# Kernel tuning notes

Measured on AMD Instinct MI355X. Metric: run time of the kernel, lower is better.

## Reference

```python
import jax, jax.numpy as jnp
import numpy as np

LN_EPS = 1e-5


def layer_norm(x, w, b):
    mu = jnp.mean(x, axis=-1, keepdims=True)
    var = jnp.mean(jnp.square(x - mu), axis=-1, keepdims=True)
    return (x - mu) * jax.lax.rsqrt(var + LN_EPS) * w + b


def setup_inputs() -> dict:
    key = jax.random.key(0)
    ks = jax.random.split(key, 10)
    B, S, D, H, DH, F = 2, 2048, 1024, 16, 64, 4096

    def xavier(k, shape):
        fan_in, fan_out = shape[-1], int(np.prod(shape[:-1]))
        lim = float(np.sqrt(6.0 / (fan_in + fan_out)))
        return jax.random.uniform(k, shape, jnp.float32, -lim, lim)

    x = jax.random.normal(ks[0], (B, S, D), jnp.float32)
    W_Q = xavier(ks[1], (H, DH, D))
    W_K = xavier(ks[2], (H, DH, D))
    W_V = xavier(ks[3], (H, DH, D))
    W_O = xavier(ks[4], (D, DH, H))
    mlp_w1 = jax.random.normal(ks[5], (F, D), jnp.float32) * (1.0 / np.sqrt(D))
    mlp_b1 = jnp.zeros((F,), jnp.float32)
    mlp_w2 = jax.random.normal(ks[6], (D, F), jnp.float32) * (1.0 / np.sqrt(F))
    mlp_b2 = jnp.zeros((D,), jnp.float32)
    ln_att_w = jnp.ones((D,), jnp.float32)
    ln_att_b = jnp.zeros((D,), jnp.float32)
    ln_mlp_w = jnp.ones((D,), jnp.float32)
    ln_mlp_b = jnp.zeros((D,), jnp.float32)
    return dict(x=x, W_Q=W_Q, W_K=W_K, W_V=W_V, W_O=W_O,
                ln_att_w=ln_att_w, ln_att_b=ln_att_b,
                ln_mlp_w=ln_mlp_w, ln_mlp_b=ln_mlp_b,
                mlp_w1=mlp_w1, mlp_b1=mlp_b1, mlp_w2=mlp_w2, mlp_b2=mlp_b2)


def reference(x, W_Q, W_K, W_V, W_O, ln_att_w, ln_att_b, ln_mlp_w, ln_mlp_b,
              mlp_w1, mlp_b1, mlp_w2, mlp_b2):
    B, S, D = x.shape
    d_head = W_Q.shape[1]
    y = layer_norm(x, ln_att_w, ln_att_b)
    Q = jnp.einsum('ihd,bpd->biph', W_Q, y)  # [B,H,S,dh]
    K = jnp.einsum('ihd,bpd->biph', W_K, y)
    V = jnp.einsum('ihd,bpd->biph', W_V, y)
    scores = jnp.einsum('biph,biqh->biqp', K, Q)  # [B,H,q,p]
    causal = jnp.tril(jnp.ones((S, S), jnp.bool_))  # True where attended
    masked = scores - 1e10 * (~causal).astype(scores.dtype)
    att = jax.nn.softmax(masked / np.sqrt(d_head), axis=-1)
    z = jnp.einsum('biph,biqp->biqh', V, att)
    x_att = jnp.einsum('dhi,biqh->bqd', W_O, z)
    x = x + x_att
    y2 = layer_norm(x, ln_mlp_w, ln_mlp_b)
    h = jax.nn.relu(y2 @ mlp_w1.T + mlp_b1)
    x = x + (h @ mlp_w2.T + mlp_b2)
    return x, att
```

## Files before the change

### kernel.cpp

```cpp
#include <hip/hip_runtime.h>
#include <hip/hip_bf16.h>
#include <stdint.h>

typedef __attribute__((ext_vector_type(8))) short bf16x8;
typedef __attribute__((ext_vector_type(4))) short short4v;
typedef __attribute__((ext_vector_type(4))) float f32x4;

#define GLOAD16(g, s) __builtin_amdgcn_global_load_lds( \
    (const __attribute__((address_space(1))) void*)(g),  \
    (__attribute__((address_space(3))) void*)(s), 16, 0, 0)

static __device__ __forceinline__ short f2bf(float f) {
  unsigned u = __builtin_bit_cast(unsigned, f);
  u += 0x7fffu + ((u >> 16) & 1u);
  return (short)(u >> 16);
}

static __device__ __forceinline__ f32x4 mfma16(bf16x8 a, bf16x8 b, f32x4 c) {
  return __builtin_amdgcn_mfma_f32_16x16x32_bf16(a, b, c, 0, 0, 0);
}

__global__ __launch_bounds__(256) void cvt_all(
    const float* __restrict__ WQ, const float* __restrict__ WK,
    const float* __restrict__ WV, const float* __restrict__ WO,
    const float* __restrict__ w1, const float* __restrict__ w2,
    short* __restrict__ Wqkv, short* __restrict__ Wob,
    short* __restrict__ w1b, short* __restrict__ w2b) {
  const int bi = blockIdx.x, tid = threadIdx.x;
  if (bi < 3072) {
    const float* src = bi < 1024 ? WQ : (bi < 2048 ? WK : WV);
    const float4 v = ((const float4*)(src + (size_t)(bi & 1023) * 1024))[tid];
    short4v o;
    o[0] = f2bf(v.x); o[1] = f2bf(v.y); o[2] = f2bf(v.z); o[3] = f2bf(v.w);
    ((short4v*)(Wqkv + (size_t)bi * 1024))[tid] = o;
  } else if (bi < 7168) {
    const int i = (bi - 3072) * 256 + tid;
    const float4 v = ((const float4*)w1)[i];
    short4v o;
    o[0] = f2bf(v.x); o[1] = f2bf(v.y); o[2] = f2bf(v.z); o[3] = f2bf(v.w);
    ((short4v*)w1b)[i] = o;
  } else if (bi < 11264) {
    const int i = (bi - 7168) * 256 + tid;
    const float4 v = ((const float4*)w2)[i];
    short4v o;
    o[0] = f2bf(v.x); o[1] = f2bf(v.y); o[2] = f2bf(v.z); o[3] = f2bf(v.w);
    ((short4v*)w2b)[i] = o;
  } else {
    const int idx = (bi - 11264) * 256 + tid;
    const int d = idx >> 10, cc = idx & 1023;
    const int i = cc >> 6, h = cc & 63;
    Wob[idx] = f2bf(WO[((size_t)d * 64 + h) * 16 + i]);
  }
}

__global__ __launch_bounds__(256) void ln_kernel(const float* __restrict__ x,
                                                 const float* __restrict__ w,
                                                 const float* __restrict__ b,
                                                 short* __restrict__ y) {
  const int row = blockIdx.x, tid = threadIdx.x;
  const int lane = tid & 63, wave = tid >> 6;
  const float4 xv = *(const float4*)&x[(size_t)row * 1024 + tid * 4];
  float s1 = xv.x + xv.y + xv.z + xv.w;
  float s2 = xv.x * xv.x + xv.y * xv.y + xv.z * xv.z + xv.w * xv.w;
#pragma unroll
  for (int off = 1; off < 64; off <<= 1) {
    s1 += __shfl_xor(s1, off);
    s2 += __shfl_xor(s2, off);
  }
  __shared__ float red[8];
  if (lane == 0) { red[wave] = s1; red[4 + wave] = s2; }
  __syncthreads();
  s1 = red[0] + red[1] + red[2] + red[3];
  s2 = red[4] + red[5] + red[6] + red[7];
  const float mu = s1 * (1.0f / 1024.0f);
  const float var = s2 * (1.0f / 1024.0f) - mu * mu;
  const float rs = rsqrtf(var + 1e-5f);
  const float4 wv = *(const float4*)&w[tid * 4];
  const float4 bv = *(const float4*)&b[tid * 4];
  short4v o;
  o[0] = f2bf((xv.x - mu) * rs * wv.x + bv.x);
  o[1] = f2bf((xv.y - mu) * rs * wv.y + bv.y);
  o[2] = f2bf((xv.z - mu) * rs * wv.z + bv.z);
  o[3] = f2bf((xv.w - mu) * rs * wv.w + bv.w);
  *(short4v*)&y[(size_t)row * 1024 + tid * 4] = o;
}

template <int MODE, int BM, int BN>
__global__ __launch_bounds__(256) void gemm_bf16k(
    const short* __restrict__ A, const short* __restrict__ Bw,
    float* __restrict__ outF, short* __restrict__ outB,
    const float* __restrict__ resid, const float* __restrict__ bias,
    int M, int N, int K) {
  constexpr int RBM = BM / 2, RBN = BN / 2;
  constexpr int FM = RBM / 16, FN = RBN / 16;
  constexpr int TCA = BM / 8, TCB = BN / 8, TC = TCA + TCB;
  __shared__ short As[BM * 64];
  __shared__ short Bs[BN * 64];
  const int tid = threadIdx.x, lane = tid & 63, wave = tid >> 6;
  const int nbx = gridDim.x, nwg = nbx * gridDim.y;
  int lid = (int)blockIdx.y * nbx + (int)blockIdx.x;
  lid = (lid & 7) * (nwg >> 3) + (lid >> 3);
  const int m0 = (lid / nbx) * BM, n0 = (lid % nbx) * BN;
  const int wm = (wave & 1) * RBM, wn = (wave >> 1) * RBN;
  const int lr = lane >> 3;
  const int lc = (lane & 7) * 8;
  f32x4 acc[FM][FN] = {};

  for (int kt = 0; kt < K; kt += 64) {
#pragma unroll
    for (int i = 0; i < TC / 4; ++i) {
      const int ch = i * 4 + wave;
      if (ch < TCA) {
        const short* ga = A + (size_t)(m0 + ch * 8 + lr) * K + kt + lc;
        GLOAD16(ga, &As[ch * 512]);
      } else {
        const int cb = ch - TCA;
        const short* gb = Bw + (size_t)(n0 + cb * 8 + lr) * K + kt + lc;
        GLOAD16(gb, &Bs[cb * 512]);
      }
    }
    __syncthreads();
#pragma unroll
    for (int kk = 0; kk < 64; kk += 32) {
      bf16x8 af[FM], bfr[FN];
#pragma unroll
      for (int i2 = 0; i2 < FM; ++i2)
        af[i2] = *(const bf16x8*)&As[(wm + i2 * 16 + (lane & 15)) * 64 + kk + (lane >> 4) * 8];
#pragma unroll
      for (int j2 = 0; j2 < FN; ++j2)
        bfr[j2] = *(const bf16x8*)&Bs[(wn + j2 * 16 + (lane & 15)) * 64 + kk + (lane >> 4) * 8];
#pragma unroll
      for (int i2 = 0; i2 < FM; ++i2)
#pragma unroll
        for (int j2 = 0; j2 < FN; ++j2)
          acc[i2][j2] = mfma16(af[i2], bfr[j2], acc[i2][j2]);
    }
    __syncthreads();
  }

#pragma unroll
  for (int i2 = 0; i2 < FM; ++i2)
#pragma unroll
    for (int j2 = 0; j2 < FN; ++j2)
#pragma unroll
      for (int r = 0; r < 4; ++r) {
        const int m = m0 + wm + i2 * 16 + (lane >> 4) * 4 + r;
        const int n = n0 + wn + j2 * 16 + (lane & 15);
        const float v = acc[i2][j2][r];
        if (MODE == 0) {
          const size_t oi = (size_t)(n >> 10) * 4194304 +
              ((size_t)((m >> 11) * 16 + ((n & 1023) >> 6)) * 2048 + (m & 2047)) * 64 +
              (n & 63);
          outB[oi] = f2bf(v);
        } else if (MODE == 1) {
          outF[(size_t)m * N + n] = resid[(size_t)m * N + n] + v;
        } else if (MODE == 2) {
          const float t2 = v + bias[n];
          outB[(size_t)m * N + n] = f2bf(t2 > 0.0f ? t2 : 0.0f);
        } else {
          outF[(size_t)m * N + n] = resid[(size_t)m * N + n] + v + bias[n];
        }
      }
}

__global__ __launch_bounds__(256) void transpose_v(const short* __restrict__ V,
                                                   short* __restrict__ Vt) {
  __shared__ short t[64][72];
  const int bi = blockIdx.y;
  const int p0 = blockIdx.x * 64;
  const short* Vh = V + (size_t)bi * 2048 * 64;
  short* Vth = Vt + (size_t)bi * 64 * 2048;
  const int tid = threadIdx.x;
  {
    const int pr = tid >> 2, h0 = (tid & 3) * 16;
    const bf16x8* src = (const bf16x8*)&Vh[(size_t)(p0 + pr) * 64 + h0];
    bf16x8 v0 = src[0], v1 = src[1];
#pragma unroll
    for (int j = 0; j < 8; ++j) { t[pr][h0 + j] = v0[j]; t[pr][h0 + 8 + j] = v1[j]; }
  }
  __syncthreads();
  {
    const int hr = tid >> 2, pq = (tid & 3) * 16;
    bf16x8 o0, o1;
#pragma unroll
    for (int j = 0; j < 8; ++j) { o0[j] = t[pq + j][hr]; o1[j] = t[pq + 8 + j][hr]; }
    *(bf16x8*)&Vth[(size_t)hr * 2048 + p0 + pq] = o0;
    *(bf16x8*)&Vth[(size_t)hr * 2048 + p0 + pq + 8] = o1;
  }
}

__global__ __launch_bounds__(256, 2) void attn_flash(
    const short* __restrict__ Q, const short* __restrict__ K,
    const short* __restrict__ Vt, float* __restrict__ ml,
    short* __restrict__ zb) {
  __shared__ __align__(16) char smem[34816];
  const int tid = threadIdx.x, lane = tid & 63, pc = tid >> 6;
  const int g = lane >> 4, c = lane & 15;
  const int qt = 63 - (int)blockIdx.x;
  const int bi = blockIdx.y;
  const int b = bi >> 4, hd = bi & 15;
  const size_t hoff = (size_t)bi * 2048 * 64;
  const short* Qh = Q + hoff;
  const short* Kh = K + hoff;
  const short* Vth = Vt + hoff;
  short* zbh = zb + (size_t)b * 2048 * 1024 + hd * 64;

  const int qw = qt * 32;
  const int P = qw + 32;
  const int csz = ((P + 511) >> 9) << 7;
  const int p_lo = pc * csz;
  const int p_hi = min(p_lo + csz, P);

  short* pbuf = (short*)smem + pc * 4224;
  float* mlb  = (float*)(smem + 33792);
  float* zm   = (float*)smem;

  const bf16x8* qp0 = (const bf16x8*)&Qh[(size_t)(qw + c) * 64];
  const bf16x8* qp1 = (const bf16x8*)&Qh[(size_t)(qw + 16 + c) * 64];
  bf16x8 aq[2][2];
  aq[0][0] = qp0[g]; aq[0][1] = qp0[4 + g];
  aq[1][0] = qp1[g]; aq[1][1] = qp1[4 + g];

  float m4[2][4], l4[2][4];
  f32x4 zacc[2][4] = {};
#pragma unroll
  for (int rb = 0; rb < 2; ++rb)
#pragma unroll
    for (int r = 0; r < 4; ++r) { m4[rb][r] = -1e30f; l4[rb][r] = 0.0f; }

  for (int p0 = p_lo; p0 < p_hi; p0 += 128) {
    bf16x8 k0[8], k1[8];
#pragma unroll
    for (int kb = 0; kb < 8; ++kb) {
      int row = p0 + kb * 16 + c;
      row = row < 2047 ? row : 2047;
      const bf16x8* kp = (const bf16x8*)&Kh[(size_t)row * 64];
      k0[kb] = kp[g]; k1[kb] = kp[4 + g];
    }
    const bool needmask = (p0 + 128 > qw);
#pragma unroll
    for (int rb = 0; rb < 2; ++rb) {
      f32x4 s[8];
#pragma unroll
      for (int kb = 0; kb < 8; ++kb) {
        f32x4 z4 = {0.0f, 0.0f, 0.0f, 0.0f};
        z4 = mfma16(aq[rb][0], k0[kb], z4);
        s[kb] = mfma16(aq[rb][1], k1[kb], z4);
      }
#pragma unroll
      for (int r = 0; r < 4; ++r) {
        const int q = qw + rb * 16 + g * 4 + r;
        float v[8];
        if (needmask) {
#pragma unroll
          for (int kb = 0; kb < 8; ++kb)
            v[kb] = (p0 + kb * 16 + c <= q) ? s[kb][r] * 0.125f : -1e30f;
        } else {
#pragma unroll
          for (int kb = 0; kb < 8; ++kb) v[kb] = s[kb][r] * 0.125f;
        }
        float mx = fmaxf(fmaxf(fmaxf(v[0], v[1]), fmaxf(v[2], v[3])),
                         fmaxf(fmaxf(v[4], v[5]), fmaxf(v[6], v[7])));
#pragma unroll
        for (int off = 1; off < 16; off <<= 1)
          mx = fmaxf(mx, __shfl_xor(mx, off));
        const float mn = fmaxf(m4[rb][r], mx);
        const float fac = __expf(m4[rb][r] - mn);
        m4[rb][r] = mn;
        float lsum = 0.0f;
        if (needmask) {
#pragma unroll
          for (int kb = 0; kb < 8; ++kb) {
            const int p = p0 + kb * 16 + c;
            const float e = (p <= q) ? __expf(v[kb] - mn) : 0.0f;
            lsum += e;
            pbuf[(rb * 16 + g * 4 + r) * 132 + kb * 16 + c] = f2bf(e);
          }
        } else {
#pragma unroll
          for (int kb = 0; kb < 8; ++kb) {
            const float e = __expf(v[kb] - mn);
            lsum += e;
            pbuf[(rb * 16 + g * 4 + r) * 132 + kb * 16 + c] = f2bf(e);
          }
        }
        l4[rb][r] = l4[rb][r] * fac + lsum;
#pragma unroll
        for (int hb = 0; hb < 4; ++hb) zacc[rb][hb][r] *= fac;
      }
    }
#pragma unroll
    for (int j = 0; j < 4; ++j) {
      const short4v p0lo = *(const short4v*)&pbuf[c * 132 + j * 32 + g * 8];
      const short4v p0hi = *(const short4v*)&pbuf[c * 132 + j * 32 + g * 8 + 4];
      const short4v p1lo = *(const short4v*)&pbuf[(16 + c) * 132 + j * 32 + g * 8];
      const short4v p1hi = *(const short4v*)&pbuf[(16 + c) * 132 + j * 32 + g * 8 + 4];
      const bf16x8 pa0 = __builtin_shufflevector(p0lo, p0hi, 0, 1, 2, 3, 4, 5, 6, 7);
      const bf16x8 pa1 = __builtin_shufflevector(p1lo, p1hi, 0, 1, 2, 3, 4, 5, 6, 7);
#pragma unroll
      for (int hb = 0; hb < 4; ++hb) {
        const bf16x8 bv =
            *(const bf16x8*)&Vth[(size_t)(hb * 16 + c) * 2048 + p0 + j * 32 + g * 8];
        zacc[0][hb] = mfma16(pa0, bv, zacc[0][hb]);
        zacc[1][hb] = mfma16(pa1, bv, zacc[1][hb]);
      }
    }
  }

#pragma unroll
  for (int rb = 0; rb < 2; ++rb)
#pragma unroll
    for (int r = 0; r < 4; ++r)
#pragma unroll
      for (int off = 1; off < 16; off <<= 1)
        l4[rb][r] += __shfl_xor(l4[rb][r], off);

  if (c == 0) {
#pragma unroll
    for (int rb = 0; rb < 2; ++rb)
#pragma unroll
      for (int r = 0; r < 4; ++r) {
        mlb[(pc * 32 + rb * 16 + g * 4 + r) * 2 + 0] = m4[rb][r];
        mlb[(pc * 32 + rb * 16 + g * 4 + r) * 2 + 1] = l4[rb][r];
      }
  }
  __syncthreads();

  if (pc != 0) {
#pragma unroll
    for (int rb = 0; rb < 2; ++rb)
#pragma unroll
      for (int hb = 0; hb < 4; ++hb)
#pragma unroll
        for (int r = 0; r < 4; ++r)
          zm[((pc - 1) * 32 + rb * 16 + g * 4 + r) * 68 + hb * 16 + c] = zacc[rb][hb][r];
  }
  __syncthreads();
  if (pc == 0) {
#pragma unroll
    for (int rb = 0; rb < 2; ++rb)
#pragma unroll
      for (int r = 0; r < 4; ++r) {
        const int row = rb * 16 + g * 4 + r;
        float M = -1e30f;
#pragma unroll
        for (int j = 0; j < 4; ++j) M = fmaxf(M, mlb[(j * 32 + row) * 2 + 0]);
        float w[4], L = 0.0f;
#pragma unroll
        for (int j = 0; j < 4; ++j) {
          w[j] = __expf(mlb[(j * 32 + row) * 2 + 0] - M);
          L += mlb[(j * 32 + row) * 2 + 1] * w[j];
        }
        const float iL = 1.0f / L;
#pragma unroll
        for (int hb = 0; hb < 4; ++hb) {
          float z = zacc[rb][hb][r] * w[0];
#pragma unroll
          for (int j = 1; j < 4; ++j)
            z += zm[((j - 1) * 32 + row) * 68 + hb * 16 + c] * w[j];
          zbh[(size_t)(qw + row) * 1024 + hb * 16 + c] = f2bf(z * iL);
        }
        if (c == 0)
          ((float2*)ml)[(size_t)bi * 2048 + qw + row] = make_float2(M, iL);
      }
  }
}

__global__ __launch_bounds__(256) void att_write(
    const short* __restrict__ Q, const short* __restrict__ K,
    const float* __restrict__ ml, float* __restrict__ att) {
  __shared__ float fbuf_s[4][16 * 36];
  const int tid = threadIdx.x, lane = tid & 63, wave = tid >> 6;
  const int g = lane >> 4, c = lane & 15;
  const int qt = blockIdx.x, pt = blockIdx.y, bi = blockIdx.z;
  const int qs = wave >> 1, ph = wave & 1;
  const int qw = qt * 32 + qs * 16;
  const int pb = pt * 256 + ph * 128;
  float* atth = att + (size_t)bi * 2048 * 2048;
  const int r0 = lane >> 3, c4 = (lane & 7) * 4;

  if (pb > qw + 15) {
    const f32x4 zf = {0.0f, 0.0f, 0.0f, 0.0f};
#pragma unroll
    for (int j = 0; j < 4; ++j) {
      __builtin_nontemporal_store(zf, (f32x4*)&atth[(size_t)(qw + r0) * 2048 + pb + j * 32 + c4]);
      __builtin_nontemporal_store(zf, (f32x4*)&atth[(size_t)(qw + 8 + r0) * 2048 + pb + j * 32 + c4]);
    }
    return;
  }

  const size_t hoff = (size_t)bi * 2048 * 64;
  const short* Qh = Q + hoff;
  const short* Kh = K + hoff;
  const bf16x8* qp = (const bf16x8*)&Qh[(size_t)(qw + c) * 64];
  const bf16x8 aq0 = qp[g], aq1 = qp[4 + g];
  float m4[4], il[4];
#pragma unroll
  for (int r = 0; r < 4; ++r) {
    const float2 t = ((const float2*)ml)[(size_t)bi * 2048 + qw + g * 4 + r];
    m4[r] = t.x; il[r] = t.y;
  }
  float* fbuf = fbuf_s[wave];
  for (int p0 = pb; p0 < pb + 128; p0 += 32) {
    const bf16x8* kp0 = (const bf16x8*)&Kh[(size_t)(p0 + c) * 64];
    const bf16x8* kp1 = (const bf16x8*)&Kh[(size_t)(p0 + 16 + c) * 64];
    f32x4 s0 = {0.0f, 0.0f, 0.0f, 0.0f}, s1 = {0.0f, 0.0f, 0.0f, 0.0f};
    s0 = mfma16(aq0, kp0[g], s0);
    s0 = mfma16(aq1, kp0[4 + g], s0);
    s1 = mfma16(aq0, kp1[g], s1);
    s1 = mfma16(aq1, kp1[4 + g], s1);
#pragma unroll
    for (int f = 0; f < 2; ++f) {
      const f32x4& ss = f ? s1 : s0;
#pragma unroll
      for (int r = 0; r < 4; ++r) {
        const int q = qw + g * 4 + r, p = p0 + f * 16 + c;
        const float e = (p <= q) ? __expf(ss[r] * 0.125f - m4[r]) * il[r] : 0.0f;
        fbuf[(g * 4 + r) * 36 + f * 16 + c] = e;
      }
    }
    const f32x4 v0 = *(const f32x4*)&fbuf[r0 * 36 + c4];
    const f32x4 v1 = *(const f32x4*)&fbuf[(8 + r0) * 36 + c4];
    __builtin_nontemporal_store(v0, (f32x4*)&atth[(size_t)(qw + r0) * 2048 + p0 + c4]);
    __builtin_nontemporal_store(v1, (f32x4*)&atth[(size_t)(qw + 8 + r0) * 2048 + p0 + c4]);
  }
}

extern "C" void kernel_launch(void* const* d_in, const int* in_sizes, int n_in,
                              void* d_out, int out_size, void* d_ws, size_t ws_size,
                              hipStream_t stream) {
  (void)in_sizes; (void)n_in; (void)out_size; (void)ws_size;
  const float* x    = (const float*)d_in[0];
  const float* WQ   = (const float*)d_in[1];
  const float* WK   = (const float*)d_in[2];
  const float* WV   = (const float*)d_in[3];
  const float* WO   = (const float*)d_in[4];
  const float* lnaw = (const float*)d_in[5];
  const float* lnab = (const float*)d_in[6];
  const float* lnmw = (const float*)d_in[7];
  const float* lnmb = (const float*)d_in[8];
  const float* w1   = (const float*)d_in[9];
  const float* b1   = (const float*)d_in[10];
  const float* w2   = (const float*)d_in[11];
  const float* b2   = (const float*)d_in[12];

  char* ws = (char*)d_ws;
  const size_t MB = 1024 * 1024;
  short* Wqkv = (short*)(ws + 0 * MB);
  short* Wob  = (short*)(ws + 6 * MB);
  short* w1b  = (short*)(ws + 8 * MB);
  short* w2b  = (short*)(ws + 16 * MB);
  short* yb   = (short*)(ws + 24 * MB);
  short* Qb   = (short*)(ws + 32 * MB);
  short* Kb   = (short*)(ws + 40 * MB);
  short* Vb   = (short*)(ws + 48 * MB);
  short* Vtb  = (short*)(ws + 56 * MB);
  short* zbuf = (short*)(ws + 64 * MB);
  float* x1   = (float*)(ws + 72 * MB);
  float* mlw  = (float*)(ws + 72 * MB);
  short* hb   = (short*)(ws + 32 * MB);

  float* outx = (float*)d_out;
  float* att  = outx + (size_t)2 * 2048 * 1024;

  cvt_all<<<dim3(15360), dim3(256), 0, stream>>>(WQ, WK, WV, WO, w1, w2,
                                                 Wqkv, Wob, w1b, w2b);

  ln_kernel<<<dim3(4096), dim3(256), 0, stream>>>(x, lnaw, lnab, yb);

  gemm_bf16k<0, 128, 128><<<dim3(24, 32), dim3(256), 0, stream>>>(
      yb, Wqkv, nullptr, Qb, nullptr, nullptr, 4096, 3072, 1024);

  transpose_v<<<dim3(32, 32), dim3(256), 0, stream>>>(Vb, Vtb);

  attn_flash<<<dim3(64, 32), dim3(256), 0, stream>>>(Qb, Kb, Vtb, mlw, zbuf);

  att_write<<<dim3(64, 8, 32), dim3(256), 0, stream>>>(Qb, Kb, mlw, att);

  gemm_bf16k<1, 128, 64><<<dim3(16, 32), dim3(256), 0, stream>>>(
      zbuf, Wob, x1, nullptr, x, nullptr, 4096, 1024, 1024);

  ln_kernel<<<dim3(4096), dim3(256), 0, stream>>>(x1, lnmw, lnmb, yb);

  gemm_bf16k<2, 128, 128><<<dim3(32, 32), dim3(256), 0, stream>>>(
      yb, w1b, nullptr, hb, nullptr, b1, 4096, 4096, 1024);
  gemm_bf16k<3, 128, 64><<<dim3(16, 32), dim3(256), 0, stream>>>(
      hb, w2b, outx, nullptr, x1, b2, 4096, 1024, 4096);
}
```

Baseline: 467.0 us.

## Merge launches: fuse LN into weight prep, run W_O GEMM alongside attention write

Folds the first layer norm into the weight-conversion kernel as extra blocks, and merges the W_O projection GEMM with the attention-probability write kernel into one launch. The GEMM's 512 tiles come first in the grid, followed by the att_write blocks, which share one dynamic-sized shared buffer. The ml buffer moves so it no longer aliases x1, which is now written concurrently. This removes launch gaps and lets the compute-bound GEMM overlap the bandwidth-bound att write, at the cost of a larger shared-memory footprint for att_write blocks and a branchy mixed kernel.

```diff
diff --git a/kernel.cpp b/kernel.cpp
--- a/kernel.cpp
+++ b/kernel.cpp
@@ -20,12 +20,102 @@
   return __builtin_amdgcn_mfma_f32_16x16x32_bf16(a, b, c, 0, 0, 0);
 }
 
-__global__ __launch_bounds__(256) void cvt_all(
+template <int MODE, int BM, int BN>
+static __device__ __forceinline__ void gemm_body(
+    int lid, int nbx,
+    const short* __restrict__ A, const short* __restrict__ Bw,
+    float* __restrict__ outF, short* __restrict__ outB,
+    const float* __restrict__ resid, const float* __restrict__ bias,
+    int M, int N, int K, short* As, short* Bs) {
+  constexpr int RBM = BM / 2, RBN = BN / 2;
+  constexpr int FM = RBM / 16, FN = RBN / 16;
+  constexpr int TCA = BM / 8, TCB = BN / 8, TC = TCA + TCB;
+  const int tid = threadIdx.x, lane = tid & 63, wave = tid >> 6;
+  const int m0 = (lid / nbx) * BM, n0 = (lid % nbx) * BN;
+  const int wm = (wave & 1) * RBM, wn = (wave >> 1) * RBN;
+  const int lr = lane >> 3;
+  const int lc = (lane & 7) * 8;
+  f32x4 acc[FM][FN] = {};
+
+  for (int kt = 0; kt < K; kt += 64) {
+#pragma unroll
+    for (int i = 0; i < TC / 4; ++i) {
+      const int ch = i * 4 + wave;
+      if (ch < TCA) {
+        GLOAD16(A + (size_t)(m0 + ch * 8 + lr) * K + kt + lc, &As[ch * 512]);
+      } else {
+        const int cb = ch - TCA;
+        GLOAD16(Bw + (size_t)(n0 + cb * 8 + lr) * K + kt + lc, &Bs[cb * 512]);
+      }
+    }
+    __syncthreads();
+#pragma unroll
+    for (int kk = 0; kk < 64; kk += 32) {
+      bf16x8 af[FM], bfr[FN];
+#pragma unroll
+      for (int i2 = 0; i2 < FM; ++i2)
+        af[i2] = *(const bf16x8*)&As[(wm + i2 * 16 + (lane & 15)) * 64 + kk + (lane >> 4) * 8];
+#pragma unroll
+      for (int j2 = 0; j2 < FN; ++j2)
+        bfr[j2] = *(const bf16x8*)&Bs[(wn + j2 * 16 + (lane & 15)) * 64 + kk + (lane >> 4) * 8];
+#pragma unroll
+      for (int i2 = 0; i2 < FM; ++i2)
+#pragma unroll
+        for (int j2 = 0; j2 < FN; ++j2)
+          acc[i2][j2] = mfma16(af[i2], bfr[j2], acc[i2][j2]);
+    }
+    __syncthreads();
+  }
+
+#pragma unroll
+  for (int i2 = 0; i2 < FM; ++i2)
+#pragma unroll
+    for (int j2 = 0; j2 < FN; ++j2)
+#pragma unroll
+      for (int r = 0; r < 4; ++r) {
+        const int m = m0 + wm + i2 * 16 + (lane >> 4) * 4 + r;
+        const int n = n0 + wn + j2 * 16 + (lane & 15);
+        const float v = acc[i2][j2][r];
+        if (MODE == 0) {
+          const size_t oi = (size_t)(n >> 10) * 4194304 +
+              ((size_t)((m >> 11) * 16 + ((n & 1023) >> 6)) * 2048 + (m & 2047)) * 64 +
+              (n & 63);
+          outB[oi] = f2bf(v);
+        } else if (MODE == 1) {
+          outF[(size_t)m * N + n] = resid[(size_t)m * N + n] + v;
+        } else if (MODE == 2) {
+          const float t2 = v + bias[n];
+          outB[(size_t)m * N + n] = f2bf(t2 > 0.0f ? t2 : 0.0f);
+        } else {
+          outF[(size_t)m * N + n] = resid[(size_t)m * N + n] + v + bias[n];
+        }
+      }
+}
+
+template <int MODE, int BM, int BN>
+__global__ __launch_bounds__(256) void gemm_bf16k(
+    const short* __restrict__ A, const short* __restrict__ Bw,
+    float* __restrict__ outF, short* __restrict__ outB,
+    const float* __restrict__ resid, const float* __restrict__ bias,
+    int M, int N, int K) {
+  __shared__ short As[BM * 64];
+  __shared__ short Bs[BN * 64];
+  const int nbx = gridDim.x, nwg = nbx * gridDim.y;
+  int lid = (int)blockIdx.y * nbx + (int)blockIdx.x;
+  lid = (lid & 7) * (nwg >> 3) + (lid >> 3);
+  gemm_body<MODE, BM, BN>(lid, nbx, A, Bw, outF, outB, resid, bias, M, N, K, As, Bs);
+}
+
+__global__ __launch_bounds__(256) void prep_all(
     const float* __restrict__ WQ, const float* __restrict__ WK,
     const float* __restrict__ WV, const float* __restrict__ WO,
     const float* __restrict__ w1, const float* __restrict__ w2,
+    const float* __restrict__ x, const float* __restrict__ lnw,
+    const float* __restrict__ lnb,
     short* __restrict__ Wqkv, short* __restrict__ Wob,
-    short* __restrict__ w1b, short* __restrict__ w2b) {
+    short* __restrict__ w1b, short* __restrict__ w2b,
+    short* __restrict__ yb) {
+  __shared__ float red[8];
   const int bi = blockIdx.x, tid = threadIdx.x;
   if (bi < 3072) {
     const float* src = bi < 1024 ? WQ : (bi < 2048 ? WK : WV);
@@ -45,11 +135,37 @@
     short4v o;
     o[0] = f2bf(v.x); o[1] = f2bf(v.y); o[2] = f2bf(v.z); o[3] = f2bf(v.w);
     ((short4v*)w2b)[i] = o;
-  } else {
+  } else if (bi < 15360) {
     const int idx = (bi - 11264) * 256 + tid;
     const int d = idx >> 10, cc = idx & 1023;
     const int i = cc >> 6, h = cc & 63;
     Wob[idx] = f2bf(WO[((size_t)d * 64 + h) * 16 + i]);
+  } else {
+    const int row = bi - 15360;
+    const int lane = tid & 63, wave = tid >> 6;
+    const float4 xv = *(const float4*)&x[(size_t)row * 1024 + tid * 4];
+    float s1 = xv.x + xv.y + xv.z + xv.w;
+    float s2 = xv.x * xv.x + xv.y * xv.y + xv.z * xv.z + xv.w * xv.w;
+#pragma unroll
+    for (int off = 1; off < 64; off <<= 1) {
+      s1 += __shfl_xor(s1, off);
+      s2 += __shfl_xor(s2, off);
+    }
+    if (lane == 0) { red[wave] = s1; red[4 + wave] = s2; }
+    __syncthreads();
+    s1 = red[0] + red[1] + red[2] + red[3];
+    s2 = red[4] + red[5] + red[6] + red[7];
+    const float mu = s1 * (1.0f / 1024.0f);
+    const float var = s2 * (1.0f / 1024.0f) - mu * mu;
+    const float rs = rsqrtf(var + 1e-5f);
+    const float4 wv = *(const float4*)&lnw[tid * 4];
+    const float4 bv = *(const float4*)&lnb[tid * 4];
+    short4v o;
+    o[0] = f2bf((xv.x - mu) * rs * wv.x + bv.x);
+    o[1] = f2bf((xv.y - mu) * rs * wv.y + bv.y);
+    o[2] = f2bf((xv.z - mu) * rs * wv.z + bv.z);
+    o[3] = f2bf((xv.w - mu) * rs * wv.w + bv.w);
+    *(short4v*)&yb[(size_t)row * 1024 + tid * 4] = o;
   }
 }
 
@@ -85,84 +201,6 @@
   *(short4v*)&y[(size_t)row * 1024 + tid * 4] = o;
 }
 
-template <int MODE, int BM, int BN>
-__global__ __launch_bounds__(256) void gemm_bf16k(
-    const short* __restrict__ A, const short* __restrict__ Bw,
-    float* __restrict__ outF, short* __restrict__ outB,
-    const float* __restrict__ resid, const float* __restrict__ bias,
-    int M, int N, int K) {
-  constexpr int RBM = BM / 2, RBN = BN / 2;
-  constexpr int FM = RBM / 16, FN = RBN / 16;
-  constexpr int TCA = BM / 8, TCB = BN / 8, TC = TCA + TCB;
-  __shared__ short As[BM * 64];
-  __shared__ short Bs[BN * 64];
-  const int tid = threadIdx.x, lane = tid & 63, wave = tid >> 6;
-  const int nbx = gridDim.x, nwg = nbx * gridDim.y;
-  int lid = (int)blockIdx.y * nbx + (int)blockIdx.x;
-  lid = (lid & 7) * (nwg >> 3) + (lid >> 3);
-  const int m0 = (lid / nbx) * BM, n0 = (lid % nbx) * BN;
-  const int wm = (wave & 1) * RBM, wn = (wave >> 1) * RBN;
-  const int lr = lane >> 3;
-  const int lc = (lane & 7) * 8;
-  f32x4 acc[FM][FN] = {};
-
-  for (int kt = 0; kt < K; kt += 64) {
-#pragma unroll
-    for (int i = 0; i < TC / 4; ++i) {
-      const int ch = i * 4 + wave;
-      if (ch < TCA) {
-        const short* ga = A + (size_t)(m0 + ch * 8 + lr) * K + kt + lc;
-        GLOAD16(ga, &As[ch * 512]);
-      } else {
-        const int cb = ch - TCA;
-        const short* gb = Bw + (size_t)(n0 + cb * 8 + lr) * K + kt + lc;
-        GLOAD16(gb, &Bs[cb * 512]);
-      }
-    }
-    __syncthreads();
-#pragma unroll
-    for (int kk = 0; kk < 64; kk += 32) {
-      bf16x8 af[FM], bfr[FN];
-#pragma unroll
-      for (int i2 = 0; i2 < FM; ++i2)
-        af[i2] = *(const bf16x8*)&As[(wm + i2 * 16 + (lane & 15)) * 64 + kk + (lane >> 4) * 8];
-#pragma unroll
-      for (int j2 = 0; j2 < FN; ++j2)
-        bfr[j2] = *(const bf16x8*)&Bs[(wn + j2 * 16 + (lane & 15)) * 64 + kk + (lane >> 4) * 8];
-#pragma unroll
-      for (int i2 = 0; i2 < FM; ++i2)
-#pragma unroll
-        for (int j2 = 0; j2 < FN; ++j2)
-          acc[i2][j2] = mfma16(af[i2], bfr[j2], acc[i2][j2]);
-    }
-    __syncthreads();
-  }
-
-#pragma unroll
-  for (int i2 = 0; i2 < FM; ++i2)
-#pragma unroll
-    for (int j2 = 0; j2 < FN; ++j2)
-#pragma unroll
-      for (int r = 0; r < 4; ++r) {
-        const int m = m0 + wm + i2 * 16 + (lane >> 4) * 4 + r;
-        const int n = n0 + wn + j2 * 16 + (lane & 15);
-        const float v = acc[i2][j2][r];
-        if (MODE == 0) {
-          const size_t oi = (size_t)(n >> 10) * 4194304 +
-              ((size_t)((m >> 11) * 16 + ((n & 1023) >> 6)) * 2048 + (m & 2047)) * 64 +
-              (n & 63);
-          outB[oi] = f2bf(v);
-        } else if (MODE == 1) {
-          outF[(size_t)m * N + n] = resid[(size_t)m * N + n] + v;
-        } else if (MODE == 2) {
-          const float t2 = v + bias[n];
-          outB[(size_t)m * N + n] = f2bf(t2 > 0.0f ? t2 : 0.0f);
-        } else {
-          outF[(size_t)m * N + n] = resid[(size_t)m * N + n] + v + bias[n];
-        }
-      }
-}
-
 __global__ __launch_bounds__(256) void transpose_v(const short* __restrict__ V,
                                                    short* __restrict__ Vt) {
   __shared__ short t[64][72];
@@ -366,13 +404,24 @@
   }
 }
 
-__global__ __launch_bounds__(256) void att_write(
+__global__ __launch_bounds__(256) void fused_wo_attw(
+    const short* __restrict__ zbuf, const short* __restrict__ Wob,
+    float* __restrict__ x1, const float* __restrict__ x,
     const short* __restrict__ Q, const short* __restrict__ K,
     const float* __restrict__ ml, float* __restrict__ att) {
-  __shared__ float fbuf_s[4][16 * 36];
+  __shared__ __align__(16) char sm[24576];
+  if (blockIdx.x < 512) {
+    gemm_body<1, 128, 64>((int)blockIdx.x, 16, zbuf, Wob, x1, nullptr, x,
+                          nullptr, 4096, 1024, 1024, (short*)sm,
+                          (short*)sm + 128 * 64);
+    return;
+  }
+  const int id = (int)blockIdx.x - 512;
+  const int bi = id >> 9;
+  const int rem = id & 511;
+  const int qt = rem >> 3, pt = rem & 7;
   const int tid = threadIdx.x, lane = tid & 63, wave = tid >> 6;
   const int g = lane >> 4, c = lane & 15;
-  const int qt = blockIdx.x, pt = blockIdx.y, bi = blockIdx.z;
   const int qs = wave >> 1, ph = wave & 1;
   const int qw = qt * 32 + qs * 16;
   const int pb = pt * 256 + ph * 128;
@@ -400,7 +449,7 @@
     const float2 t = ((const float2*)ml)[(size_t)bi * 2048 + qw + g * 4 + r];
     m4[r] = t.x; il[r] = t.y;
   }
-  float* fbuf = fbuf_s[wave];
+  float* fbuf = (float*)sm + wave * 576;
   for (int p0 = pb; p0 < pb + 128; p0 += 32) {
     const bf16x8* kp0 = (const bf16x8*)&Kh[(size_t)(p0 + c) * 64];
     const bf16x8* kp1 = (const bf16x8*)&Kh[(size_t)(p0 + 16 + c) * 64];
@@ -457,16 +506,14 @@
   short* Vtb  = (short*)(ws + 56 * MB);
   short* zbuf = (short*)(ws + 64 * MB);
   float* x1   = (float*)(ws + 72 * MB);
-  float* mlw  = (float*)(ws + 72 * MB);
+  float* mlw  = (float*)(ws + 88 * MB);
   short* hb   = (short*)(ws + 32 * MB);
 
   float* outx = (float*)d_out;
   float* att  = outx + (size_t)2 * 2048 * 1024;
 
-  cvt_all<<<dim3(15360), dim3(256), 0, stream>>>(WQ, WK, WV, WO, w1, w2,
-                                                 Wqkv, Wob, w1b, w2b);
-
-  ln_kernel<<<dim3(4096), dim3(256), 0, stream>>>(x, lnaw, lnab, yb);
+  prep_all<<<dim3(19456), dim3(256), 0, stream>>>(
+      WQ, WK, WV, WO, w1, w2, x, lnaw, lnab, Wqkv, Wob, w1b, w2b, yb);
 
   gemm_bf16k<0, 128, 128><<<dim3(24, 32), dim3(256), 0, stream>>>(
       yb, Wqkv, nullptr, Qb, nullptr, nullptr, 4096, 3072, 1024);
@@ -475,10 +522,8 @@
 
   attn_flash<<<dim3(64, 32), dim3(256), 0, stream>>>(Qb, Kb, Vtb, mlw, zbuf);
 
-  att_write<<<dim3(64, 8, 32), dim3(256), 0, stream>>>(Qb, Kb, mlw, att);
-
-  gemm_bf16k<1, 128, 64><<<dim3(16, 32), dim3(256), 0, stream>>>(
-      zbuf, Wob, x1, nullptr, x, nullptr, 4096, 1024, 1024);
+  fused_wo_attw<<<dim3(16896), dim3(256), 0, stream>>>(
+      zbuf, Wob, x1, x, Qb, Kb, mlw, att);
 
   ln_kernel<<<dim3(4096), dim3(256), 0, stream>>>(x1, lnmw, lnmb, yb);
 
```

Measured after the change: 493.1 us. +5.6%, slower.
